# Optimization experiments

Hardware: AMD Instinct MI355X
Metric: run time of the kernel (lower is better)

The kernel has to match this reference:

```python
import jax, jax.numpy as jnp
import numpy as np

B, S = 1, 1024
V_SZ, D, L, H, DK, DV = 50304, 768, 12, 24, 32, 32
EPS = 1e-5


def layernorm(x, g, b):
    m = jnp.mean(x, axis=-1, keepdims=True)
    v = jnp.mean((x - m) ** 2, axis=-1, keepdims=True)
    return (x - m) * jax.lax.rsqrt(v + EPS) * g + b


def setup_inputs() -> dict:
    key = jax.random.key(0)
    ks = jax.random.split(key, 8)
    s = 0.02
    qkv_out = H * (DK + DK + DV)
    return {
        "token_ids": jax.random.randint(ks[0], (B, S), 0, V_SZ),
        "embed_w": (jax.random.uniform(ks[1], (V_SZ, D), minval=-1.0, maxval=1.0) / np.float32(np.sqrt(D))).astype(jnp.float32),
        "pos_w": jax.random.normal(ks[2], (D, 2 * D), dtype=jnp.float32) * s,
        "pos_b": jnp.zeros((2 * D,), jnp.float32),
        "ln1_g": jnp.ones((L, D), jnp.float32),
        "ln1_b": jnp.zeros((L, D), jnp.float32),
        "qkv_w": jax.random.normal(ks[3], (L, D, qkv_out), dtype=jnp.float32) * s,
        "qkv_b": jnp.zeros((L, qkv_out), jnp.float32),
        "ff_w1": jax.random.normal(ks[4], (L, H * DV, 2 * D), dtype=jnp.float32) * s,
        "ff_b1": jnp.zeros((L, 2 * D), jnp.float32),
        "ff_w2": jax.random.normal(ks[5], (L, D, D), dtype=jnp.float32) * s,
        "lnf_g": jnp.ones((D,), jnp.float32),
        "lnf_b": jnp.zeros((D,), jnp.float32),
    }


def _embed_position(x, pos_w, pos_b):
    # Heinsen log-linear recurrence (arXiv:2311.06281), using_prev_context=False.
    h = x @ pos_w + pos_b                     # [B,S,2D]
    log_coeffs = jax.nn.log_sigmoid(h[..., :D])
    logits = h[..., D:]
    a_star = jnp.pad(jnp.cumsum(log_coeffs, axis=1), ((0, 0), (1, 0), (0, 0)))  # [B,S+1,D]
    prepended = jnp.pad(logits, ((0, 0), (1, 0), (0, 0)))                        # logit0 = 0
    rec = a_star + jax.lax.cumlogsumexp(prepended - a_star, axis=1)
    return x + rec[:, 1:, :]


def _layer(x, p):
    g1, b1, wqkv, bqkv, w1, bb1, w2 = p
    y = layernorm(x, g1, b1) @ wqkv + bqkv                  # [B,S,H*(2DK+DV)]
    y = y.reshape(B, S, H, DK + DK + DV).transpose(0, 2, 1, 3)  # [B,H,S,.]
    Q, K, V = y[..., :DK], y[..., DK:2 * DK], y[..., 2 * DK:]
    # Heinsen log-domain causal attention (arXiv:2404.05843)
    H_S = jax.lax.cumlogsumexp(K[..., :, None] + V[..., None, :], axis=2)  # [B,H,S,DK,DV]
    H_Z = jax.lax.cumlogsumexp(K, axis=2)                                   # [B,H,S,DK]
    log_S = jax.nn.logsumexp(Q[..., None] + H_S, axis=-2)                   # [B,H,S,DV]
    log_Z = jax.nn.logsumexp(Q + H_Z, axis=-1, keepdims=True)               # [B,H,S,1]
    att = (log_S - log_Z).transpose(0, 2, 1, 3).reshape(B, S, H * DV)
    z = att @ w1 + bb1                                       # [B,S,2D]
    z = z[..., :D] * jax.nn.sigmoid(z[..., D:])              # GLU(dim=-1)
    z = z @ w2
    return x + z, None


def reference(token_ids, embed_w, pos_w, pos_b, ln1_g, ln1_b, qkv_w, qkv_b, ff_w1, ff_b1, ff_w2, lnf_g, lnf_b):
    x = embed_w[token_ids]                                   # [B,S,D]
    x = _embed_position(x, pos_w, pos_b)
    x, _ = jax.lax.scan(_layer, x, (ln1_g, ln1_b, qkv_w, qkv_b, ff_w1, ff_b1, ff_w2))
    x = layernorm(x, lnf_g, lnf_b)
    return x @ embed_w.T                                     # [B,S,V_SZ]
```

## Files before the change

### kernel.cpp

```cpp
#include <hip/hip_runtime.h>
#include <math.h>

#define S 1024
#define D 768
#define L 12
#define NH 24
#define QKV_OUT 2304
#define FF1_OUT 1536
#define V_SZ 50304

typedef unsigned short u16;
typedef __attribute__((ext_vector_type(8))) short bf16x8;
typedef __attribute__((ext_vector_type(4))) float f32x4;

__device__ __forceinline__ u16 f2bf(float x) {
    unsigned u = __float_as_uint(x);
    u += 0x7fffu + ((u >> 16) & 1u);
    return (u16)(u >> 16);
}

__device__ __forceinline__ void async_copy16(const void* g, void* l) {
    __builtin_amdgcn_global_load_lds(
        (const __attribute__((address_space(1))) unsigned int*)g,
        (__attribute__((address_space(3))) unsigned int*)l, 16, 0, 0);
}

__global__ __launch_bounds__(256) void embed_kernel(
    const int* __restrict__ tok, const float* __restrict__ ew,
    float* __restrict__ x, u16* __restrict__ xb) {
    int t = blockIdx.x;
    int id = tok[t];
    const float* src = ew + (size_t)id * D;
    for (int d = threadIdx.x; d < D; d += 256) {
        float v = src[d];
        x[(size_t)t * D + d] = v;
        xb[(size_t)t * D + d] = f2bf(v);
    }
}

__global__ __launch_bounds__(256) void cvt_bf16_kernel(
    const float* __restrict__ in, u16* __restrict__ out) {
    size_t i = ((size_t)blockIdx.x * 256 + threadIdx.x) * 8;
    float4 a = *(const float4*)(in + i);
    float4 b = *(const float4*)(in + i + 4);
    uint4 o;
    o.x = (unsigned)f2bf(a.x) | ((unsigned)f2bf(a.y) << 16);
    o.y = (unsigned)f2bf(a.z) | ((unsigned)f2bf(a.w) << 16);
    o.z = (unsigned)f2bf(b.x) | ((unsigned)f2bf(b.y) << 16);
    o.w = (unsigned)f2bf(b.z) | ((unsigned)f2bf(b.w) << 16);
    *(uint4*)(out + i) = o;
}

__global__ __launch_bounds__(256) void pos_scan_kernel(
    const float* __restrict__ h, float* __restrict__ x) {
    const int d = blockIdx.x;
    const int tid = threadIdx.x;
    float a[4], b[4];
    #pragma unroll
    for (int i = 0; i < 4; ++i) {
        int t = tid * 4 + i;
        float g  = h[(size_t)t * FF1_OUT + d];
        float lg = h[(size_t)t * FF1_OUT + D + d];
        a[i] = 1.f / (1.f + __expf(-g));
        b[i] = __expf(lg);
    }
    float A = ((a[0] * a[1]) * a[2]) * a[3];
    float B = ((b[0] * a[1] + b[1]) * a[2] + b[2]) * a[3] + b[3];

    __shared__ float sA[256], sB[256];
    sA[tid] = A; sB[tid] = B;
    __syncthreads();
    #pragma unroll
    for (int off = 1; off < 256; off <<= 1) {
        float selfA = sA[tid], selfB = sB[tid];
        float pA = 1.f, pB = 0.f;
        if (tid >= off) { pA = sA[tid - off]; pB = sB[tid - off]; }
        __syncthreads();
        sA[tid] = pA * selfA;
        sB[tid] = pB * selfA + selfB;
        __syncthreads();
    }
    float R = 1.f;
    if (tid > 0) R = sA[tid - 1] + sB[tid - 1];
    #pragma unroll
    for (int i = 0; i < 4; ++i) {
        R = R * a[i] + b[i];
        x[(size_t)(tid * 4 + i) * D + d] += __logf(R);
    }
}

__global__ __launch_bounds__(256) void ln_kernel(
    const float* __restrict__ in, const float* __restrict__ g,
    const float* __restrict__ b, u16* __restrict__ out) {
    int row = blockIdx.x;
    int tid = threadIdx.x;
    const float* p = in + (size_t)row * D;
    float v0 = p[tid], v1 = p[tid + 256], v2 = p[tid + 512];

    __shared__ float red[8];
    float s = v0 + v1 + v2;
    #pragma unroll
    for (int o = 32; o > 0; o >>= 1) s += __shfl_down(s, o, 64);
    int wave = tid >> 6, lane = tid & 63;
    if (lane == 0) red[wave] = s;
    __syncthreads();
    float mean = (red[0] + red[1] + red[2] + red[3]) * (1.f / (float)D);

    float d0 = v0 - mean, d1 = v1 - mean, d2 = v2 - mean;
    float ss = d0 * d0 + d1 * d1 + d2 * d2;
    #pragma unroll
    for (int o = 32; o > 0; o >>= 1) ss += __shfl_down(ss, o, 64);
    if (lane == 0) red[4 + wave] = ss;
    __syncthreads();
    float var = (red[4] + red[5] + red[6] + red[7]) * (1.f / (float)D);
    float rstd = rsqrtf(var + 1e-5f);

    u16* o = out + (size_t)row * D;
    o[tid]       = f2bf(d0 * rstd * g[tid]       + b[tid]);
    o[tid + 256] = f2bf(d1 * rstd * g[tid + 256] + b[tid + 256]);
    o[tid + 512] = f2bf(d2 * rstd * g[tid + 512] + b[tid + 512]);
}

__global__ __launch_bounds__(256) void wconv_kernel(
    const float* __restrict__ W, u16* __restrict__ WT, int N) {
    __shared__ float tile[32][33];
    const int z = blockIdx.z;
    W  += (size_t)z * 768 * N;
    WT += (size_t)z * N * 768;
    const int n0 = blockIdx.x * 32, k0 = blockIdx.y * 32;
    const int t = threadIdx.x;
    const int r = t >> 3, c4 = (t & 7) * 4;
    float4 v = *(const float4*)(W + (size_t)(k0 + r) * N + n0 + c4);
    tile[r][c4] = v.x; tile[r][c4 + 1] = v.y; tile[r][c4 + 2] = v.z; tile[r][c4 + 3] = v.w;
    __syncthreads();
    ushort4 o;
    o.x = f2bf(tile[c4][r]);     o.y = f2bf(tile[c4 + 1][r]);
    o.z = f2bf(tile[c4 + 2][r]); o.w = f2bf(tile[c4 + 3][r]);
    *(ushort4*)(WT + (size_t)(n0 + r) * 768 + k0 + c4) = o;
}

template <bool BF16B>
__global__ __launch_bounds__(256) void gemm_kernel(
    const u16* __restrict__ A, const void* __restrict__ Bv,
    const float* __restrict__ bias, const float* __restrict__ Cin,
    float* __restrict__ C, int N) {
    constexpr int K = 768;
    __shared__ __align__(16) u16 As[128 * 32];
    __shared__ __align__(16) u16 Bs[128 * 32];
    const int tid = threadIdx.x;
    const int w = tid >> 6, lane = tid & 63;
    const int m0 = blockIdx.y * 128, n0 = blockIdx.x * 128;
    const int wm = (w >> 1) * 64, wn = (w & 1) * 64;

    f32x4 acc[4][4] = {};

    const int rA = w * 32 + (lane >> 2);
    const int cA = (lane & 3) * 8;
    const int frow = lane & 15;
    const int fko = (lane >> 4) * 8;

    for (int k0 = 0; k0 < K; k0 += 32) {
        {
            const u16* g0 = A + (size_t)(m0 + rA) * K + k0 + cA;
            async_copy16(g0, (char*)As + w * 2048);
            async_copy16(g0 + (size_t)16 * K, (char*)As + w * 2048 + 1024);
        }
        if (BF16B) {
            const u16* B = (const u16*)Bv;
            const u16* g0 = B + (size_t)(n0 + rA) * K + k0 + cA;
            async_copy16(g0, (char*)Bs + w * 2048);
            async_copy16(g0 + (size_t)16 * K, (char*)Bs + w * 2048 + 1024);
        } else {
            const float* B = (const float*)Bv;
            const int r = tid >> 1, half = tid & 1;
            const float* src = B + (size_t)(n0 + r) * K + k0 + half * 16;
            float4 v0 = *(const float4*)(src);
            float4 v1 = *(const float4*)(src + 4);
            float4 v2 = *(const float4*)(src + 8);
            float4 v3 = *(const float4*)(src + 12);
            unsigned p0 = (unsigned)f2bf(v0.x) | ((unsigned)f2bf(v0.y) << 16);
            unsigned p1 = (unsigned)f2bf(v0.z) | ((unsigned)f2bf(v0.w) << 16);
            unsigned p2 = (unsigned)f2bf(v1.x) | ((unsigned)f2bf(v1.y) << 16);
            unsigned p3 = (unsigned)f2bf(v1.z) | ((unsigned)f2bf(v1.w) << 16);
            unsigned p4 = (unsigned)f2bf(v2.x) | ((unsigned)f2bf(v2.y) << 16);
            unsigned p5 = (unsigned)f2bf(v2.z) | ((unsigned)f2bf(v2.w) << 16);
            unsigned p6 = (unsigned)f2bf(v3.x) | ((unsigned)f2bf(v3.y) << 16);
            unsigned p7 = (unsigned)f2bf(v3.z) | ((unsigned)f2bf(v3.w) << 16);
            u16* dst = Bs + r * 32 + half * 16;
            *(uint4*)(dst)     = make_uint4(p0, p1, p2, p3);
            *(uint4*)(dst + 8) = make_uint4(p4, p5, p6, p7);
        }
        __syncthreads();

        bf16x8 af[4], bfr[4];
        #pragma unroll
        for (int i = 0; i < 4; ++i)
            af[i] = *(const bf16x8*)(As + (wm + i * 16 + frow) * 32 + fko);
        #pragma unroll
        for (int j = 0; j < 4; ++j)
            bfr[j] = *(const bf16x8*)(Bs + (wn + j * 16 + frow) * 32 + fko);
        #pragma unroll
        for (int i = 0; i < 4; ++i)
            #pragma unroll
            for (int j = 0; j < 4; ++j)
                acc[i][j] = __builtin_amdgcn_mfma_f32_16x16x32_bf16(af[i], bfr[j], acc[i][j], 0, 0, 0);
        __syncthreads();
    }

    const int crow = wm + (lane >> 4) * 4;
    const int ccol = wn + (lane & 15);
    #pragma unroll
    for (int j = 0; j < 4; ++j) {
        int col = n0 + ccol + j * 16;
        float bj = bias ? bias[col] : 0.f;
        #pragma unroll
        for (int i = 0; i < 4; ++i) {
            #pragma unroll
            for (int r = 0; r < 4; ++r) {
                int row = m0 + crow + i * 16 + r;
                size_t off = (size_t)row * N + col;
                float v = acc[i][j][r] + bj;
                if (Cin) v += Cin[off];
                C[off] = v;
            }
        }
    }
}

__global__ __launch_bounds__(256) void attn_kernel(
    const float* __restrict__ y, u16* __restrict__ att) {
    const int tb = blockIdx.x, head = blockIdx.y;
    const int tid = threadIdx.x, w = tid >> 6, lane = tid & 63;
    const int q = lane >> 4, cl = lane & 15;
    const int t0 = tb * 64;

    __shared__ __align__(16) u16 Qs[64 * 32];
    __shared__ __align__(16) u16 Ks[64 * 32];
    __shared__ __align__(16) u16 Vt[32 * 64];
    __shared__ __align__(16) u16 As[4][16 * 64];
    u16* As_w = As[w];

    bf16x8 ones8;
    #pragma unroll
    for (int i = 0; i < 8; ++i) ones8[i] = (short)0x3F80;

    f32x4 accO[2] = {};
    f32x4 accZ = {};

    #pragma unroll
    for (int i = 0; i < 2; ++i) {
        int e = tid + i * 256;
        int row = e >> 3, c4 = (e & 7) * 4;
        float4 v = *(const float4*)(y + (size_t)(t0 + row) * QKV_OUT + head * 96 + c4);
        ushort4 o;
        o.x = f2bf(__expf(v.x)); o.y = f2bf(__expf(v.y));
        o.z = f2bf(__expf(v.z)); o.w = f2bf(__expf(v.w));
        *(ushort4*)(Qs + row * 32 + c4) = o;
    }

    for (int sb = 0; sb <= tb; ++sb) {
        const int s0 = sb * 64;
        #pragma unroll
        for (int i = 0; i < 2; ++i) {
            int e = tid + i * 256;
            int row = e >> 3, c4 = (e & 7) * 4;
            const float* src = y + (size_t)(s0 + row) * QKV_OUT + head * 96;
            float4 kv = *(const float4*)(src + 32 + c4);
            ushort4 o;
            o.x = f2bf(__expf(kv.x)); o.y = f2bf(__expf(kv.y));
            o.z = f2bf(__expf(kv.z)); o.w = f2bf(__expf(kv.w));
            *(ushort4*)(Ks + row * 32 + c4) = o;
            float4 vv = *(const float4*)(src + 64 + c4);
            float ev[4] = {__expf(vv.x), __expf(vv.y), __expf(vv.z), __expf(vv.w)};
            #pragma unroll
            for (int n = 0; n < 4; ++n) {
                int j = c4 + n;
                Vt[j * 64 + (((row >> 4) ^ (j & 3)) * 16) + (row & 15)] = f2bf(ev[n]);
            }
        }
        __syncthreads();

        bf16x8 af_q = *(const bf16x8*)(Qs + (w * 16 + cl) * 32 + q * 8);
        f32x4 aqk[4];
        #pragma unroll
        for (int nt = 0; nt < 4; ++nt) {
            bf16x8 bk = *(const bf16x8*)(Ks + (nt * 16 + cl) * 32 + q * 8);
            aqk[nt] = __builtin_amdgcn_mfma_f32_16x16x32_bf16(af_q, bk, (f32x4){0.f, 0.f, 0.f, 0.f}, 0, 0, 0);
        }
        #pragma unroll
        for (int nt = 0; nt < 4; ++nt) {
            #pragma unroll
            for (int reg = 0; reg < 4; ++reg) {
                int r = q * 4 + reg;
                int tg = t0 + w * 16 + r;
                int cg = s0 + nt * 16 + cl;
                float v = (cg <= tg) ? aqk[nt][reg] : 0.f;
                As_w[r * 64 + ((nt ^ q) * 16) + cl] = f2bf(v);
            }
        }
        bf16x8 af_a[2];
        #pragma unroll
        for (int kt = 0; kt < 2; ++kt) {
            int blk = (kt * 2 + (q >> 1)) ^ (cl >> 2);
            af_a[kt] = *(const bf16x8*)(As_w + cl * 64 + blk * 16 + (q & 1) * 8);
        }
        #pragma unroll
        for (int kt = 0; kt < 2; ++kt)
            accZ = __builtin_amdgcn_mfma_f32_16x16x32_bf16(af_a[kt], ones8, accZ, 0, 0, 0);
        #pragma unroll
        for (int nt = 0; nt < 2; ++nt) {
            #pragma unroll
            for (int kt = 0; kt < 2; ++kt) {
                int j = nt * 16 + cl;
                int blk = (kt * 2 + (q >> 1)) ^ (j & 3);
                bf16x8 bv = *(const bf16x8*)(Vt + j * 64 + blk * 16 + (q & 1) * 8);
                accO[nt] = __builtin_amdgcn_mfma_f32_16x16x32_bf16(af_a[kt], bv, accO[nt], 0, 0, 0);
            }
        }
        __syncthreads();
    }

    #pragma unroll
    for (int nt = 0; nt < 2; ++nt) {
        #pragma unroll
        for (int reg = 0; reg < 4; ++reg) {
            int t = t0 + w * 16 + q * 4 + reg;
            int j = nt * 16 + cl;
            att[(size_t)t * D + head * 32 + j] = f2bf(__logf(accO[nt][reg]) - __logf(accZ[reg]));
        }
    }
}

__global__ __launch_bounds__(256) void glu_kernel(
    const float* __restrict__ z, u16* __restrict__ zg) {
    int idx = blockIdx.x * 256 + threadIdx.x;
    int t = idx / D, d = idx - t * D;
    float a = z[(size_t)t * FF1_OUT + d];
    float g = z[(size_t)t * FF1_OUT + D + d];
    zg[idx] = f2bf(a * (1.f / (1.f + __expf(-g))));
}

extern "C" void kernel_launch(void* const* d_in, const int* in_sizes, int n_in,
                              void* d_out, int out_size, void* d_ws, size_t ws_size,
                              hipStream_t stream) {
    const int*   tok     = (const int*)d_in[0];
    const float* embed_w = (const float*)d_in[1];
    const float* pos_w   = (const float*)d_in[2];
    const float* pos_b   = (const float*)d_in[3];
    const float* ln1_g   = (const float*)d_in[4];
    const float* ln1_b   = (const float*)d_in[5];
    const float* qkv_w   = (const float*)d_in[6];
    const float* qkv_b   = (const float*)d_in[7];
    const float* ff_w1   = (const float*)d_in[8];
    const float* ff_b1   = (const float*)d_in[9];
    const float* ff_w2   = (const float*)d_in[10];
    const float* lnf_g   = (const float*)d_in[11];
    const float* lnf_b   = (const float*)d_in[12];
    float* out = (float*)d_out;

    char* base = (char*)d_ws;
    float* X    = (float*)(base);
    u16*   XB   = (u16*)  (base + 3145728);
    float* Y    = (float*)(base + 4718592);
    u16*   LNX  = (u16*)  (base + 14155776);
    u16*   ATT  = (u16*)  (base + 15728640);
    u16*   ZG   = (u16*)  (base + 17301504);
    u16*   posT = (u16*)  (base + 18874368);
    u16*   qkvT = (u16*)  (base + 21233664);
    u16*   ff1T = (u16*)  (base + 63700992);
    u16*   ff2T = (u16*)  (base + 92012544);
    u16*   EBW  = (u16*)  (base + 106168320);
    const bool bf16_head = ws_size >= (size_t)106168320 + 77266944;

    wconv_kernel<<<dim3(48, 24, 1),  256, 0, stream>>>(pos_w, posT, 1536);
    wconv_kernel<<<dim3(72, 24, 12), 256, 0, stream>>>(qkv_w, qkvT, 2304);
    wconv_kernel<<<dim3(48, 24, 12), 256, 0, stream>>>(ff_w1, ff1T, 1536);
    wconv_kernel<<<dim3(24, 24, 12), 256, 0, stream>>>(ff_w2, ff2T, 768);
    if (bf16_head) {
        cvt_bf16_kernel<<<18864, 256, 0, stream>>>(embed_w, EBW);
    }

    embed_kernel<<<S, 256, 0, stream>>>(tok, embed_w, X, XB);

    gemm_kernel<true><<<dim3(12, 8), 256, 0, stream>>>(XB, posT, pos_b, nullptr, Y, FF1_OUT);
    pos_scan_kernel<<<D, 256, 0, stream>>>(Y, X);

    for (int l = 0; l < L; ++l) {
        ln_kernel<<<S, 256, 0, stream>>>(X, ln1_g + (size_t)l * D, ln1_b + (size_t)l * D, LNX);
        gemm_kernel<true><<<dim3(18, 8), 256, 0, stream>>>(
            LNX, qkvT + (size_t)l * QKV_OUT * 768, qkv_b + (size_t)l * QKV_OUT, nullptr, Y, QKV_OUT);
        attn_kernel<<<dim3(16, NH), 256, 0, stream>>>(Y, ATT);
        gemm_kernel<true><<<dim3(12, 8), 256, 0, stream>>>(
            ATT, ff1T + (size_t)l * FF1_OUT * 768, ff_b1 + (size_t)l * FF1_OUT, nullptr, Y, FF1_OUT);
        glu_kernel<<<(S * D) / 256, 256, 0, stream>>>(Y, ZG);
        gemm_kernel<true><<<dim3(6, 8), 256, 0, stream>>>(
            ZG, ff2T + (size_t)l * D * 768, nullptr, X, X, D);
    }

    ln_kernel<<<S, 256, 0, stream>>>(X, lnf_g, lnf_b, LNX);
    if (bf16_head) {
        gemm_kernel<true><<<dim3(393, 8), 256, 0, stream>>>(LNX, EBW, nullptr, nullptr, out, V_SZ);
    } else {
        gemm_kernel<false><<<dim3(393, 8), 256, 0, stream>>>(LNX, embed_w, nullptr, nullptr, out, V_SZ);
    }
}
```

Baseline: 1.919 ms.

## Double-buffer LDS in bf16 GEMM and swap head grid for B-tile reuse

Adds a bf16 GEMM kernel that double-buffers the A/B LDS tiles, issuing async global-to-LDS copies for the next K-step while MFMAs run on the current one, with one barrier per iteration. For the vocab head it swaps the grid order so blocks sharing one embedding tile run back to back, which improves L2 reuse of the large weight matrix. The embed_w conversion is also moved to just before the head GEMM. Double-buffering doubles LDS use to 32KB per block, which can lower occupancy.

```diff
diff --git a/kernel.cpp b/kernel.cpp
--- a/kernel.cpp
+++ b/kernel.cpp
@@ -139,9 +139,85 @@
     *(ushort4*)(WT + (size_t)(n0 + r) * 768 + k0 + c4) = o;
 }
 
-template <bool BF16B>
-__global__ __launch_bounds__(256) void gemm_kernel(
-    const u16* __restrict__ A, const void* __restrict__ Bv,
+template <bool SWAP>
+__global__ __launch_bounds__(256) void gemm_bf16_kernel(
+    const u16* __restrict__ A, const u16* __restrict__ B,
+    const float* __restrict__ bias, const float* __restrict__ Cin,
+    float* __restrict__ C, int N) {
+    constexpr int K = 768;
+    constexpr int NT = K / 32;
+    __shared__ __align__(16) u16 As[2][128 * 32];
+    __shared__ __align__(16) u16 Bs[2][128 * 32];
+    const int tid = threadIdx.x;
+    const int w = tid >> 6, lane = tid & 63;
+    const int m0 = (SWAP ? blockIdx.x : blockIdx.y) * 128;
+    const int n0 = (SWAP ? blockIdx.y : blockIdx.x) * 128;
+    const int wm = (w >> 1) * 64, wn = (w & 1) * 64;
+
+    f32x4 acc[4][4] = {};
+
+    const int rA = w * 32 + (lane >> 2);
+    const int cA = (lane & 3) * 8;
+    const int frow = lane & 15;
+    const int fko = (lane >> 4) * 8;
+
+    const u16* gA = A + (size_t)(m0 + rA) * K + cA;
+    const u16* gB = B + (size_t)(n0 + rA) * K + cA;
+
+    async_copy16(gA, (char*)As[0] + w * 2048);
+    async_copy16(gA + (size_t)16 * K, (char*)As[0] + w * 2048 + 1024);
+    async_copy16(gB, (char*)Bs[0] + w * 2048);
+    async_copy16(gB + (size_t)16 * K, (char*)Bs[0] + w * 2048 + 1024);
+    __syncthreads();
+
+    int cur = 0;
+    for (int t = 0; t < NT; ++t) {
+        if (t + 1 < NT) {
+            const u16* a1 = gA + (t + 1) * 32;
+            const u16* b1 = gB + (t + 1) * 32;
+            async_copy16(a1, (char*)As[cur ^ 1] + w * 2048);
+            async_copy16(a1 + (size_t)16 * K, (char*)As[cur ^ 1] + w * 2048 + 1024);
+            async_copy16(b1, (char*)Bs[cur ^ 1] + w * 2048);
+            async_copy16(b1 + (size_t)16 * K, (char*)Bs[cur ^ 1] + w * 2048 + 1024);
+        }
+        bf16x8 af[4], bfr[4];
+        #pragma unroll
+        for (int i = 0; i < 4; ++i)
+            af[i] = *(const bf16x8*)(As[cur] + (wm + i * 16 + frow) * 32 + fko);
+        #pragma unroll
+        for (int j = 0; j < 4; ++j)
+            bfr[j] = *(const bf16x8*)(Bs[cur] + (wn + j * 16 + frow) * 32 + fko);
+        #pragma unroll
+        for (int i = 0; i < 4; ++i)
+            #pragma unroll
+            for (int j = 0; j < 4; ++j)
+                acc[i][j] = __builtin_amdgcn_mfma_f32_16x16x32_bf16(af[i], bfr[j], acc[i][j], 0, 0, 0);
+        __syncthreads();
+        cur ^= 1;
+    }
+
+    const int crow = wm + (lane >> 4) * 4;
+    const int ccol = wn + (lane & 15);
+    #pragma unroll
+    for (int j = 0; j < 4; ++j) {
+        int col = n0 + ccol + j * 16;
+        float bj = bias ? bias[col] : 0.f;
+        #pragma unroll
+        for (int i = 0; i < 4; ++i) {
+            #pragma unroll
+            for (int r = 0; r < 4; ++r) {
+                int row = m0 + crow + i * 16 + r;
+                size_t off = (size_t)row * N + col;
+                float v = acc[i][j][r] + bj;
+                if (Cin) v += Cin[off];
+                C[off] = v;
+            }
+        }
+    }
+}
+
+__global__ __launch_bounds__(256) void gemm_f32b_kernel(
+    const u16* __restrict__ A, const float* __restrict__ B,
     const float* __restrict__ bias, const float* __restrict__ Cin,
     float* __restrict__ C, int N) {
     constexpr int K = 768;
@@ -165,13 +241,7 @@
             async_copy16(g0, (char*)As + w * 2048);
             async_copy16(g0 + (size_t)16 * K, (char*)As + w * 2048 + 1024);
         }
-        if (BF16B) {
-            const u16* B = (const u16*)Bv;
-            const u16* g0 = B + (size_t)(n0 + rA) * K + k0 + cA;
-            async_copy16(g0, (char*)Bs + w * 2048);
-            async_copy16(g0 + (size_t)16 * K, (char*)Bs + w * 2048 + 1024);
-        } else {
-            const float* B = (const float*)Bv;
+        {
             const int r = tid >> 1, half = tid & 1;
             const float* src = B + (size_t)(n0 + r) * K + k0 + half * 16;
             float4 v0 = *(const float4*)(src);
@@ -376,31 +446,29 @@
     wconv_kernel<<<dim3(72, 24, 12), 256, 0, stream>>>(qkv_w, qkvT, 2304);
     wconv_kernel<<<dim3(48, 24, 12), 256, 0, stream>>>(ff_w1, ff1T, 1536);
     wconv_kernel<<<dim3(24, 24, 12), 256, 0, stream>>>(ff_w2, ff2T, 768);
+
+    embed_kernel<<<S, 256, 0, stream>>>(tok, embed_w, X, XB);
+
+    gemm_bf16_kernel<false><<<dim3(12, 8), 256, 0, stream>>>(XB, posT, pos_b, nullptr, Y, FF1_OUT);
+    pos_scan_kernel<<<D, 256, 0, stream>>>(Y, X);
+
+    for (int l = 0; l < L; ++l) {
+        ln_kernel<<<S, 256, 0, stream>>>(X, ln1_g + (size_t)l * D, ln1_b + (size_t)l * D, LNX);
+        gemm_bf16_kernel<false><<<dim3(18, 8), 256, 0, stream>>>(
+            LNX, qkvT + (size_t)l * QKV_OUT * 768, qkv_b + (size_t)l * QKV_OUT, nullptr, Y, QKV_OUT);
+        attn_kernel<<<dim3(16, NH), 256, 0, stream>>>(Y, ATT);
+        gemm_bf16_kernel<false><<<dim3(12, 8), 256, 0, stream>>>(
+            ATT, ff1T + (size_t)l * FF1_OUT * 768, ff_b1 + (size_t)l * FF1_OUT, nullptr, Y, FF1_OUT);
+        glu_kernel<<<(S * D) / 256, 256, 0, stream>>>(Y, ZG);
+        gemm_bf16_kernel<false><<<dim3(6, 8), 256, 0, stream>>>(
+            ZG, ff2T + (size_t)l * D * 768, nullptr, X, X, D);
+    }
+
+    ln_kernel<<<S, 256, 0, stream>>>(X, lnf_g, lnf_b, LNX);
     if (bf16_head) {
         cvt_bf16_kernel<<<18864, 256, 0, stream>>>(embed_w, EBW);
-    }
-
-    embed_kernel<<<S, 256, 0, stream>>>(tok, embed_w, X, XB);
-
-    gemm_kernel<true><<<dim3(12, 8), 256, 0, stream>>>(XB, posT, pos_b, nullptr, Y, FF1_OUT);
-    pos_scan_kernel<<<D, 256, 0, stream>>>(Y, X);
-
-    for (int l = 0; l < L; ++l) {
-        ln_kernel<<<S, 256, 0, stream>>>(X, ln1_g + (size_t)l * D, ln1_b + (size_t)l * D, LNX);
-        gemm_kernel<true><<<dim3(18, 8), 256, 0, stream>>>(
-            LNX, qkvT + (size_t)l * QKV_OUT * 768, qkv_b + (size_t)l * QKV_OUT, nullptr, Y, QKV_OUT);
-        attn_kernel<<<dim3(16, NH), 256, 0, stream>>>(Y, ATT);
-        gemm_kernel<true><<<dim3(12, 8), 256, 0, stream>>>(
-            ATT, ff1T + (size_t)l * FF1_OUT * 768, ff_b1 + (size_t)l * FF1_OUT, nullptr, Y, FF1_OUT);
-        glu_kernel<<<(S * D) / 256, 256, 0, stream>>>(Y, ZG);
-        gemm_kernel<true><<<dim3(6, 8), 256, 0, stream>>>(
-            ZG, ff2T + (size_t)l * D * 768, nullptr, X, X, D);
-    }
-
-    ln_kernel<<<S, 256, 0, stream>>>(X, lnf_g, lnf_b, LNX);
-    if (bf16_head) {
-        gemm_kernel<true><<<dim3(393, 8), 256, 0, stream>>>(LNX, EBW, nullptr, nullptr, out, V_SZ);
+        gemm_bf16_kernel<true><<<dim3(8, 393), 256, 0, stream>>>(LNX, EBW, nullptr, nullptr, out, V_SZ);
     } else {
-        gemm_kernel<false><<<dim3(393, 8), 256, 0, stream>>>(LNX, embed_w, nullptr, nullptr, out, V_SZ);
-    }
-}
+        gemm_f32b_kernel<<<dim3(393, 8), 256, 0, stream>>>(LNX, embed_w, nullptr, nullptr, out, V_SZ);
+    }
+}
```

Result: no change. 1.926 ms (+0.4%).
